# Kernel optimization log

Hardware: AMD Instinct MI355X
Metric: run time of the kernel (lower is better)

## Reference

```python
import jax, jax.numpy as jnp
import numpy as np

H = 1024

def setup_inputs() -> dict:
    key = jax.random.key(0)
    k1, k2, k3, k4, k5 = jax.random.split(key, 5)
    B, T = 32, 2048
    s = 1.0 / np.sqrt(H)
    return {
        "decoder_state": jax.random.normal(k1, (B, H), dtype=jnp.float32),
        "encoder_states": jax.random.normal(k2, (B, T, H), dtype=jnp.float32),
        "Wa_w": jax.random.uniform(k3, (H, H), jnp.float32, -s, s),
        "Wa_b": jnp.zeros((H,), jnp.float32),
        "Ua_w": jax.random.uniform(k4, (H, H), jnp.float32, -s, s),
        "Ua_b": jnp.zeros((H,), jnp.float32),
        "v_w": jax.random.uniform(k5, (H,), jnp.float32, -s, s),
        "v_b": jnp.zeros((), jnp.float32),
    }

def reference(decoder_state, encoder_states, Wa_w, Wa_b, Ua_w, Ua_b, v_w, v_b):
    # decoder_state: [B,H], encoder_states: [B,T,H]
    dec_proj = decoder_state @ Ua_w.T + Ua_b            # [B,H]
    enc_proj = jnp.einsum('bth,oh->bto', encoder_states, Wa_w) + Wa_b  # [B,T,H]
    e = jnp.tanh(dec_proj[:, None, :] + enc_proj)        # [B,T,H]
    scores = jnp.einsum('bth,h->bt', e, v_w) + v_b       # [B,T]
    attn_weights = jax.nn.softmax(scores, axis=1)        # [B,T]
    context = jnp.einsum('bt,bth->bh', attn_weights, encoder_states)  # [B,H]
    return (context, attn_weights)
```

## Files before the change

### kernel.cpp

```cpp
#include <hip/hip_runtime.h>
#include <hip/hip_bf16.h>

#define HH 1024
#define BB 32
#define TT 2048

typedef __attribute__((ext_vector_type(8))) short bf16x8;
typedef __attribute__((ext_vector_type(4))) float f32x4;

static __device__ __forceinline__ unsigned short f2bf(float f) {
    unsigned int u = __float_as_uint(f);
    unsigned int r = u + 0x7fffu + ((u >> 16) & 1u);
    return (unsigned short)(r >> 16);
}
static __device__ __forceinline__ unsigned int cvt_pk_bf16(float lo, float hi) {
    unsigned int d;
    asm volatile("v_cvt_pk_bf16_f32 %0, %1, %2" : "=v"(d) : "v"(lo), "v"(hi));
    return d;
}
static __device__ __forceinline__ float fast_tanh(float x) {
    float e = __expf(2.0f * x);
    return 1.0f - 2.0f / (e + 1.0f);
}

#define GLOAD_LDS16(gp, lp) \
    __builtin_amdgcn_global_load_lds( \
        (const __attribute__((address_space(1))) void*)(gp), \
        (__attribute__((address_space(3))) void*)(lp), 16, 0, 0)

__global__ void k_convW(const float* __restrict__ W, unsigned short* __restrict__ Wb) {
    int i = blockIdx.x * 256 + threadIdx.x;
    float4 v = ((const float4*)W)[i];
    ushort4 o;
    o.x = f2bf(v.x); o.y = f2bf(v.y); o.z = f2bf(v.z); o.w = f2bf(v.w);
    ((ushort4*)Wb)[i] = o;
}

__global__ void k_decproj(const float* __restrict__ dec, const float* __restrict__ Ua,
                          const float* __restrict__ Uab, const float* __restrict__ Wab,
                          float* __restrict__ dp) {
    int gtid = blockIdx.x * 256 + threadIdx.x;
    int b = gtid >> 10, o = gtid & 1023;
    const float4* d4 = (const float4*)(dec + (long)b * HH);
    const float4* u4 = (const float4*)(Ua + (long)o * HH);
    float acc = 0.f;
    for (int k = 0; k < HH / 4; ++k) {
        float4 a = d4[k], w = u4[k];
        acc += a.x * w.x + a.y * w.y + a.z * w.z + a.w * w.w;
    }
    dp[gtid] = acc + Uab[o] + Wab[o];
}

__global__ __launch_bounds__(512) void k_score_bf(
        const float* __restrict__ enc, const unsigned short* __restrict__ Wb,
        const float* __restrict__ dp, const float* __restrict__ vw,
        float* __restrict__ scores) {
    __shared__ __align__(16) unsigned short As[2][256 * 64];
    __shared__ __align__(16) unsigned short Bs[2][256 * 64];
    int bid = blockIdx.x;
    int xcd = bid & 7;
    int ord = bid >> 3;
    int nt = ord & 3;
    int mt = (ord >> 2) * 8 + xcd;
    long m0 = (long)mt * 256;
    int o0b = nt * 256;
    int tid = threadIdx.x;
    int lane = tid & 63, wid = tid >> 6;
    int wm = wid >> 2, wn = wid & 3;
    int r = lane & 15, g = lane >> 4;

    f32x4 acc[8][4];
    #pragma unroll
    for (int i = 0; i < 8; ++i)
        #pragma unroll
        for (int j = 0; j < 4; ++j) acc[i][j] = (f32x4){0.f, 0.f, 0.f, 0.f};

    int srow = tid >> 3;
    int acol = (tid & 7) * 8;
    int awu = (tid & 7) ^ (srow & 7);
    const float* aSrcF = enc + (m0 + srow) * HH + acol;
    const unsigned short* bSrc = Wb + (long)(o0b + srow) * HH + awu * 8;
    int ldso = wid * 512;
    int rx = r & 7;
    int u0 = (g ^ rx) * 8;
    int u1 = ((4 + g) ^ rx) * 8;
    int aw0 = srow * 64 + awu * 8;

    float4 ar[8];

    {
        float4 a0[8];
        #pragma unroll
        for (int q = 0; q < 4; ++q) {
            a0[2 * q]     = *(const float4*)(aSrcF + (long)64 * q * HH);
            a0[2 * q + 1] = *(const float4*)(aSrcF + (long)64 * q * HH + 4);
            GLOAD_LDS16(bSrc + (long)q * 64 * HH, &Bs[0][ldso + q * 4096]);
        }
        #pragma unroll
        for (int q = 0; q < 4; ++q) {
            uint4 w;
            w.x = cvt_pk_bf16(a0[2 * q].x, a0[2 * q].y);
            w.y = cvt_pk_bf16(a0[2 * q].z, a0[2 * q].w);
            w.z = cvt_pk_bf16(a0[2 * q + 1].x, a0[2 * q + 1].y);
            w.w = cvt_pk_bf16(a0[2 * q + 1].z, a0[2 * q + 1].w);
            *(uint4*)(&As[0][aw0 + q * 4096]) = w;
        }
        #pragma unroll
        for (int q = 0; q < 4; ++q) {
            ar[2 * q]     = *(const float4*)(aSrcF + (long)64 * q * HH + 64);
            ar[2 * q + 1] = *(const float4*)(aSrcF + (long)64 * q * HH + 64 + 4);
        }
        asm volatile("s_waitcnt vmcnt(8)" ::: "memory");
        asm volatile("s_waitcnt lgkmcnt(0)" ::: "memory");
        __builtin_amdgcn_s_barrier();
        __builtin_amdgcn_sched_barrier(0);
    }

    #pragma unroll 1
    for (int t = 0; t < 16; ++t) {
        int bi = t & 1, pi = bi ^ 1;
        int kc2 = (t + 1) * 64;
        bool pre = (t < 15);

        bf16x8 bfr[4][2];
        #pragma unroll
        for (int ni = 0; ni < 4; ++ni) {
            int rowb = (wn * 64 + ni * 16 + r) * 64;
            bfr[ni][0] = *(const bf16x8*)(&Bs[bi][rowb + u0]);
            bfr[ni][1] = *(const bf16x8*)(&Bs[bi][rowb + u1]);
        }
        bf16x8 aq[2][2][2];
        #pragma unroll
        for (int q = 0; q < 2; ++q) {
            int rowa = (wm * 128 + q * 16 + r) * 64;
            aq[0][q][0] = *(const bf16x8*)(&As[bi][rowa + u0]);
            aq[0][q][1] = *(const bf16x8*)(&As[bi][rowa + u1]);
        }

        #pragma unroll
        for (int p = 0; p < 4; ++p) {
            if (pre && p == 0) {
                GLOAD_LDS16(bSrc + kc2 + (long)0 * 64 * HH, &Bs[pi][ldso + 0 * 4096]);
                GLOAD_LDS16(bSrc + kc2 + (long)1 * 64 * HH, &Bs[pi][ldso + 1 * 4096]);
            }
            if (pre && p == 1) {
                GLOAD_LDS16(bSrc + kc2 + (long)2 * 64 * HH, &Bs[pi][ldso + 2 * 4096]);
                GLOAD_LDS16(bSrc + kc2 + (long)3 * 64 * HH, &Bs[pi][ldso + 3 * 4096]);
            }
            if (p < 3) {
                #pragma unroll
                for (int q = 0; q < 2; ++q) {
                    int rowa = (wm * 128 + (2 * (p + 1) + q) * 16 + r) * 64;
                    aq[(p + 1) & 1][q][0] = *(const bf16x8*)(&As[bi][rowa + u0]);
                    aq[(p + 1) & 1][q][1] = *(const bf16x8*)(&As[bi][rowa + u1]);
                }
            }
            __builtin_amdgcn_s_setprio(1);
            #pragma unroll
            for (int q = 0; q < 2; ++q) {
                int mi = 2 * p + q;
                #pragma unroll
                for (int ni = 0; ni < 4; ++ni) {
                    acc[mi][ni] = __builtin_amdgcn_mfma_f32_16x16x32_bf16(
                        aq[p & 1][q][0], bfr[ni][0], acc[mi][ni], 0, 0, 0);
                    acc[mi][ni] = __builtin_amdgcn_mfma_f32_16x16x32_bf16(
                        aq[p & 1][q][1], bfr[ni][1], acc[mi][ni], 0, 0, 0);
                }
            }
            __builtin_amdgcn_s_setprio(0);
        }

        if (pre) {
            #pragma unroll
            for (int q = 0; q < 4; ++q) {
                uint4 w;
                w.x = cvt_pk_bf16(ar[2 * q].x, ar[2 * q].y);
                w.y = cvt_pk_bf16(ar[2 * q].z, ar[2 * q].w);
                w.z = cvt_pk_bf16(ar[2 * q + 1].x, ar[2 * q + 1].y);
                w.w = cvt_pk_bf16(ar[2 * q + 1].z, ar[2 * q + 1].w);
                *(uint4*)(&As[pi][aw0 + q * 4096]) = w;
            }
        }
        if (t < 14) {
            int kc3 = (t + 2) * 64;
            #pragma unroll
            for (int q = 0; q < 4; ++q) {
                ar[2 * q]     = *(const float4*)(aSrcF + (long)64 * q * HH + kc3);
                ar[2 * q + 1] = *(const float4*)(aSrcF + (long)64 * q * HH + kc3 + 4);
            }
            asm volatile("s_waitcnt vmcnt(8)" ::: "memory");
        } else if (t == 14) {
            asm volatile("s_waitcnt vmcnt(0)" ::: "memory");
        }
        if (pre) {
            asm volatile("s_waitcnt lgkmcnt(0)" ::: "memory");
            __builtin_amdgcn_s_barrier();
            __builtin_amdgcn_sched_barrier(0);
        }
    }

    int bb = (int)(m0 >> 11);
    float vv[4], dpv[4];
    #pragma unroll
    for (int ni = 0; ni < 4; ++ni) {
        int o = o0b + wn * 64 + ni * 16 + r;
        vv[ni] = vw[o];
        dpv[ni] = dp[bb * HH + o];
    }
    #pragma unroll
    for (int mi = 0; mi < 8; ++mi) {
        float vp[4] = {0.f, 0.f, 0.f, 0.f};
        #pragma unroll
        for (int ni = 0; ni < 4; ++ni)
            #pragma unroll
            for (int j = 0; j < 4; ++j)
                vp[j] += fast_tanh(acc[mi][ni][j] + dpv[ni]) * vv[ni];
        #pragma unroll
        for (int j = 0; j < 4; ++j) {
            float s = vp[j];
            s += __shfl_xor(s, 1); s += __shfl_xor(s, 2);
            s += __shfl_xor(s, 4); s += __shfl_xor(s, 8);
            if (r == 0) {
                int row = wm * 128 + mi * 16 + g * 4 + j;
                atomicAdd(&scores[m0 + row], s);
            }
        }
    }
}

__global__ void k_softmax(float* __restrict__ w) {
    int b = blockIdx.x;
    float* row = w + (long)b * TT;
    int tid = threadIdx.x;
    float loc[8];
    float m = -1e30f;
    #pragma unroll
    for (int i = 0; i < 8; ++i) { loc[i] = row[tid + i * 256]; m = fmaxf(m, loc[i]); }
    #pragma unroll
    for (int off = 1; off < 64; off <<= 1) m = fmaxf(m, __shfl_xor(m, off));
    __shared__ float red[4];
    if ((tid & 63) == 0) red[tid >> 6] = m;
    __syncthreads();
    m = fmaxf(fmaxf(red[0], red[1]), fmaxf(red[2], red[3]));
    float s = 0.f;
    #pragma unroll
    for (int i = 0; i < 8; ++i) { loc[i] = __expf(loc[i] - m); s += loc[i]; }
    #pragma unroll
    for (int off = 1; off < 64; off <<= 1) s += __shfl_xor(s, off);
    __shared__ float red2[4];
    if ((tid & 63) == 0) red2[tid >> 6] = s;
    __syncthreads();
    s = red2[0] + red2[1] + red2[2] + red2[3];
    float inv = 1.0f / s;
    #pragma unroll
    for (int i = 0; i < 8; ++i) row[tid + i * 256] = loc[i] * inv;
}

__global__ void k_context(const float* __restrict__ enc, const float* __restrict__ w,
                          float* __restrict__ ctx) {
    int bid = blockIdx.x;
    int b = bid >> 6;
    int hc = (bid >> 4) & 3;
    int ts = bid & 15;
    int h = hc * 256 + threadIdx.x;
    const float* wr = w + (long)b * TT + ts * 128;
    long base = ((long)b * TT + (long)ts * 128) * HH + h;
    float acc = 0.f;
    #pragma unroll 4
    for (int t = 0; t < 128; ++t)
        acc += wr[t] * enc[base + (long)t * HH];
    atomicAdd(&ctx[b * HH + h], acc);
}

extern "C" void kernel_launch(void* const* d_in, const int* in_sizes, int n_in,
                              void* d_out, int out_size, void* d_ws, size_t ws_size,
                              hipStream_t stream) {
    const float* dec  = (const float*)d_in[0];
    const float* enc  = (const float*)d_in[1];
    const float* Wa_w = (const float*)d_in[2];
    const float* Wa_b = (const float*)d_in[3];
    const float* Ua_w = (const float*)d_in[4];
    const float* Ua_b = (const float*)d_in[5];
    const float* v_w  = (const float*)d_in[6];

    float* out  = (float*)d_out;
    float* ctx  = out;
    float* attn = out + BB * HH;

    float* dpw = (float*)d_ws;
    unsigned short* Wb = (unsigned short*)((char*)d_ws + 131072);

    hipMemsetAsync(d_out, 0, (size_t)out_size * sizeof(float), stream);
    k_convW<<<1024, 256, 0, stream>>>(Wa_w, Wb);
    k_decproj<<<128, 256, 0, stream>>>(dec, Ua_w, Ua_b, Wa_b, dpw);
    k_score_bf<<<1024, 512, 0, stream>>>(enc, Wb, dpw, v_w, attn);
    k_softmax<<<BB, 256, 0, stream>>>(attn);
    k_context<<<2048, 256, 0, stream>>>(enc, attn, ctx);
}
```

Before: 262.3 us.

## Emit bf16 copy of encoder states from score GEMM for context pass

```diff
diff --git a/kernel.cpp b/kernel.cpp
--- a/kernel.cpp
+++ b/kernel.cpp
@@ -12,6 +12,9 @@
     unsigned int u = __float_as_uint(f);
     unsigned int r = u + 0x7fffu + ((u >> 16) & 1u);
     return (unsigned short)(r >> 16);
+}
+static __device__ __forceinline__ float bf2f(unsigned short u) {
+    return __uint_as_float(((unsigned int)u) << 16);
 }
 static __device__ __forceinline__ unsigned int cvt_pk_bf16(float lo, float hi) {
     unsigned int d;
@@ -51,10 +54,11 @@
     dp[gtid] = acc + Uab[o] + Wab[o];
 }
 
+template<int WRITE_ENC>
 __global__ __launch_bounds__(512) void k_score_bf(
         const float* __restrict__ enc, const unsigned short* __restrict__ Wb,
         const float* __restrict__ dp, const float* __restrict__ vw,
-        float* __restrict__ scores) {
+        float* __restrict__ scores, unsigned short* __restrict__ encb) {
     __shared__ __align__(16) unsigned short As[2][256 * 64];
     __shared__ __align__(16) unsigned short Bs[2][256 * 64];
     int bid = blockIdx.x;
@@ -80,6 +84,7 @@
     int awu = (tid & 7) ^ (srow & 7);
     const float* aSrcF = enc + (m0 + srow) * HH + acol;
     const unsigned short* bSrc = Wb + (long)(o0b + srow) * HH + awu * 8;
+    unsigned short* eDst = WRITE_ENC ? encb + (m0 + srow) * HH + acol : nullptr;
     int ldso = wid * 512;
     int rx = r & 7;
     int u0 = (g ^ rx) * 8;
@@ -96,14 +101,19 @@
             a0[2 * q + 1] = *(const float4*)(aSrcF + (long)64 * q * HH + 4);
             GLOAD_LDS16(bSrc + (long)q * 64 * HH, &Bs[0][ldso + q * 4096]);
         }
+        uint4 wv[4];
         #pragma unroll
         for (int q = 0; q < 4; ++q) {
-            uint4 w;
-            w.x = cvt_pk_bf16(a0[2 * q].x, a0[2 * q].y);
-            w.y = cvt_pk_bf16(a0[2 * q].z, a0[2 * q].w);
-            w.z = cvt_pk_bf16(a0[2 * q + 1].x, a0[2 * q + 1].y);
-            w.w = cvt_pk_bf16(a0[2 * q + 1].z, a0[2 * q + 1].w);
-            *(uint4*)(&As[0][aw0 + q * 4096]) = w;
+            wv[q].x = cvt_pk_bf16(a0[2 * q].x, a0[2 * q].y);
+            wv[q].y = cvt_pk_bf16(a0[2 * q].z, a0[2 * q].w);
+            wv[q].z = cvt_pk_bf16(a0[2 * q + 1].x, a0[2 * q + 1].y);
+            wv[q].w = cvt_pk_bf16(a0[2 * q + 1].z, a0[2 * q + 1].w);
+            *(uint4*)(&As[0][aw0 + q * 4096]) = wv[q];
+        }
+        if (WRITE_ENC && nt == 0) {
+            #pragma unroll
+            for (int q = 0; q < 4; ++q)
+                *(uint4*)(eDst + (long)64 * q * HH) = wv[q];
         }
         #pragma unroll
         for (int q = 0; q < 4; ++q) {
@@ -171,14 +181,19 @@
         }
 
         if (pre) {
+            uint4 wv[4];
             #pragma unroll
             for (int q = 0; q < 4; ++q) {
-                uint4 w;
-                w.x = cvt_pk_bf16(ar[2 * q].x, ar[2 * q].y);
-                w.y = cvt_pk_bf16(ar[2 * q].z, ar[2 * q].w);
-                w.z = cvt_pk_bf16(ar[2 * q + 1].x, ar[2 * q + 1].y);
-                w.w = cvt_pk_bf16(ar[2 * q + 1].z, ar[2 * q + 1].w);
-                *(uint4*)(&As[pi][aw0 + q * 4096]) = w;
+                wv[q].x = cvt_pk_bf16(ar[2 * q].x, ar[2 * q].y);
+                wv[q].y = cvt_pk_bf16(ar[2 * q].z, ar[2 * q].w);
+                wv[q].z = cvt_pk_bf16(ar[2 * q + 1].x, ar[2 * q + 1].y);
+                wv[q].w = cvt_pk_bf16(ar[2 * q + 1].z, ar[2 * q + 1].w);
+                *(uint4*)(&As[pi][aw0 + q * 4096]) = wv[q];
+            }
+            if (WRITE_ENC && ((t + 1) & 3) == nt) {
+                #pragma unroll
+                for (int q = 0; q < 4; ++q)
+                    *(uint4*)(eDst + (long)64 * q * HH + kc2) = wv[q];
             }
         }
         if (t < 14) {
@@ -254,6 +269,30 @@
     float inv = 1.0f / s;
     #pragma unroll
     for (int i = 0; i < 8; ++i) row[tid + i * 256] = loc[i] * inv;
+}
+
+__global__ void k_context_bf(const unsigned short* __restrict__ encb,
+                             const float* __restrict__ w, float* __restrict__ ctx) {
+    int bid = blockIdx.x;
+    int b = bid >> 4;
+    int ts = bid & 15;
+    int h = threadIdx.x * 4;
+    const float* wr = w + (long)b * TT + ts * 128;
+    long base = ((long)b * TT + (long)ts * 128) * HH + h;
+    float a0 = 0.f, a1 = 0.f, a2 = 0.f, a3 = 0.f;
+    #pragma unroll 4
+    for (int t = 0; t < 128; ++t) {
+        ushort4 e = *(const ushort4*)(encb + base + (long)t * HH);
+        float ww = wr[t];
+        a0 += ww * bf2f(e.x);
+        a1 += ww * bf2f(e.y);
+        a2 += ww * bf2f(e.z);
+        a3 += ww * bf2f(e.w);
+    }
+    atomicAdd(&ctx[b * HH + h], a0);
+    atomicAdd(&ctx[b * HH + h + 1], a1);
+    atomicAdd(&ctx[b * HH + h + 2], a2);
+    atomicAdd(&ctx[b * HH + h + 3], a3);
 }
 
 __global__ void k_context(const float* __restrict__ enc, const float* __restrict__ w,
@@ -289,11 +328,20 @@
 
     float* dpw = (float*)d_ws;
     unsigned short* Wb = (unsigned short*)((char*)d_ws + 131072);
+    unsigned short* encb = (unsigned short*)((char*)d_ws + 131072 + 2097152);
+    const size_t NEED = 131072ull + 2097152ull + (size_t)BB * TT * HH * 2;
 
     hipMemsetAsync(d_out, 0, (size_t)out_size * sizeof(float), stream);
     k_convW<<<1024, 256, 0, stream>>>(Wa_w, Wb);
     k_decproj<<<128, 256, 0, stream>>>(dec, Ua_w, Ua_b, Wa_b, dpw);
-    k_score_bf<<<1024, 512, 0, stream>>>(enc, Wb, dpw, v_w, attn);
-    k_softmax<<<BB, 256, 0, stream>>>(attn);
-    k_context<<<2048, 256, 0, stream>>>(enc, attn, ctx);
-}
+
+    if (ws_size >= NEED) {
+        k_score_bf<1><<<1024, 512, 0, stream>>>(enc, Wb, dpw, v_w, attn, encb);
+        k_softmax<<<BB, 256, 0, stream>>>(attn);
+        k_context_bf<<<512, 256, 0, stream>>>(encb, attn, ctx);
+    } else {
+        k_score_bf<0><<<1024, 512, 0, stream>>>(enc, Wb, dpw, v_w, attn, nullptr);
+        k_softmax<<<BB, 256, 0, stream>>>(attn);
+        k_context<<<2048, 256, 0, stream>>>(enc, attn, ctx);
+    }
+}
```

After: 278.4 us. 1.06x slower.
